# Optimization experiments

Measured on AMD Instinct MI355X. Metric: run time of the kernel, lower is better.

## Reference

```python
import jax, jax.numpy as jnp
import numpy as np
from jax import lax

B, IN_CH, H, W = 512, 20, 32, 32
FEAT, NUM_AGENTS, NUM_ACTIONS = 128, 4, 16
NUM_UNIT, NUM_CITY = 12, 4


def setup_inputs() -> dict:
    key = jax.random.key(0)
    ks = jax.random.split(key, 6)
    states = jax.random.normal(ks[0], (B, IN_CH, H, W), dtype=jnp.float32)
    labels = jax.random.randint(ks[1], (B,), 0, NUM_AGENTS, dtype=jnp.int32)
    maskings = jnp.ones((B, 1, H, W), dtype=jnp.float32)
    # get_feature params: 3x3 conv trunk (stand-in for PolicyNetwork.get_feature)
    conv_w = jax.random.normal(ks[2], (FEAT, IN_CH, 3, 3), dtype=jnp.float32) * 0.05
    conv_b = jnp.zeros((FEAT,), dtype=jnp.float32)
    # Stacked per-agent heads: index 0 = policy_net.fc1, 1.. = fc_list
    W_all = jax.random.normal(ks[3], (NUM_AGENTS, NUM_ACTIONS, FEAT), dtype=jnp.float32) * 0.05
    b_all = jax.random.normal(ks[4], (NUM_AGENTS, NUM_ACTIONS), dtype=jnp.float32) * 0.05
    return {"states": states, "labels": labels, "maskings": maskings,
            "conv_w": conv_w, "conv_b": conv_b, "W_all": W_all, "b_all": b_all}


def _get_feature(states, maskings, conv_w, conv_b):
    x = lax.conv_general_dilated(states, conv_w, (1, 1), 'SAME',
                                 dimension_numbers=('NCHW', 'OIHW', 'NCHW'))
    x = jax.nn.relu(x + conv_b[None, :, None, None])
    return x * maskings  # [B, FEAT, H, W]


def reference(states, labels, maskings, conv_w, conv_b, W_all, b_all):
    x = _get_feature(states, maskings, conv_w, conv_b)
    b, c, h, w = x.shape
    x = x.transpose(0, 2, 3, 1).reshape(b, h * w, c)  # [B, HW, C]
    # Equivalent to computing all num_agents heads then gathering by label:
    # select each sample's head weights, then one batched GEMM.
    W_sel = W_all[labels]          # [B, K, C]
    b_sel = b_all[labels]          # [B, K]
    out = jnp.einsum('bnc,bkc->bnk', x, W_sel) + b_sel[:, None, :]
    out = out.reshape(b, h, w, NUM_ACTIONS)
    return out[..., :NUM_UNIT], out[..., NUM_UNIT:]
```

## Files before the change

kernel.cpp:

```cpp
#include <hip/hip_runtime.h>
#include <hip/hip_bf16.h>
#include <stdint.h>

#define BATCH   512
#define INCH    20
#define FEAT    128
#define KACT    16
#define NUNIT   12

typedef short bf16x8 __attribute__((ext_vector_type(8)));
typedef float f32x4  __attribute__((ext_vector_type(4)));

#define BPACK_ELEMS (3*2*4*128*8)
#define WHEAD_ELEMS (4*4*4*16*8)

#define XIN_ELEMS   (34*34*20 + 64)

__device__ __forceinline__ uint16_t f2bf(float f) {
    union { float f; uint32_t u; } x{f};
    uint32_t u = x.u;
    return (uint16_t)((u + 0x7FFFu + ((u >> 16) & 1u)) >> 16);
}

__device__ __forceinline__ uint32_t cvt_pk_bf16(float lo, float hi) {
    uint32_t r;
    asm("v_cvt_pk_bf16_f32 %0, %1, %2" : "=v"(r) : "v"(lo), "v"(hi));
    return r;
}

__device__ __forceinline__ void lds_barrier() {
    asm volatile("s_waitcnt lgkmcnt(0)\n\ts_barrier" ::: "memory");
}

__global__ void repack_kernel(const float* __restrict__ conv_w,
                              const float* __restrict__ W_all,
                              uint16_t* __restrict__ Bpack,
                              uint16_t* __restrict__ Whead) {
    int idx = blockIdx.x * 256 + threadIdx.x;
    if (idx < BPACK_ELEMS) {
        int j = idx & 7, t = idx >> 3;
        int f = t & 127; t >>= 7;
        int g = t & 3;   t >>= 2;
        int kk = t & 1;  int ky = t >> 1;
        int k = kk * 32 + g * 8 + j;
        float v = 0.0f;
        if (k < 60) {
            int kx = k / 20, c = k % 20;
            v = conv_w[((f * INCH + c) * 3 + ky) * 3 + kx];
        }
        Bpack[idx] = f2bf(v);
    } else if (idx < BPACK_ELEMS + WHEAD_ELEMS) {
        int i = idx - BPACK_ELEMS;
        int j = i & 7, t = i >> 3;
        int a = t & 15; t >>= 4;
        int g = t & 3;  t >>= 2;
        int kt = t & 3; int ag = t >> 2;
        int f = kt * 32 + g * 8 + j;
        Whead[i] = f2bf(W_all[(ag * KACT + a) * FEAT + f]);
    }
}

__global__ __launch_bounds__(512, 4) void fused_mfma_kernel(
    const float* __restrict__ states,
    const int*   __restrict__ labels,
    const float* __restrict__ maskings,
    const float* __restrict__ conv_b,
    const float* __restrict__ b_all,
    const uint16_t* __restrict__ Bpack,
    const uint16_t* __restrict__ Whead,
    float*       __restrict__ out)
{
    __shared__ __align__(16) uint16_t xin[XIN_ELEMS];
    __shared__ __align__(16) uint16_t xl[2 * 64 * 128];

    const int b    = blockIdx.x;
    const int tid  = threadIdx.x;
    const int lane = tid & 63;
    const int w    = tid >> 6;
    const int l15  = lane & 15;
    const int g    = lane >> 4;
    const int wr   = w >> 2;
    const int fq   = w & 3;
    const int swz  = (l15 & 7) << 4;

    for (int i = tid; i < XIN_ELEMS / 8; i += 512)
        ((uint4*)xin)[i] = uint4{0, 0, 0, 0};
    __syncthreads();

    for (int t = 0; t < 10; ++t) {
        int i  = t * 512 + tid;
        int p  = i & 1023;
        int cg = i >> 10;
        int y  = p >> 5, x = p & 31;
        const float* sp = states + (size_t)b * (INCH * 1024) + cg * 4096 + p;
        float v0 = sp[0], v1 = sp[1024], v2 = sp[2048], v3 = sp[3072];
        uint64_t lo = cvt_pk_bf16(v0, v1);
        uint64_t hi = cvt_pk_bf16(v2, v3);
        *(uint64_t*)&xin[((y + 1) * 34 + (x + 1)) * 20 + cg * 4] = lo | (hi << 32);
    }

    const int label = labels[b];
    f32x4 cb[2];
    #pragma unroll
    for (int nt = 0; nt < 2; ++nt)
        cb[nt] = *(const f32x4*)&conv_b[fq * 32 + nt * 16 + g * 4];
    const f32x4 hb = *(const f32x4*)&b_all[label * KACT + g * 4];
    bf16x8 Wh[4];
    #pragma unroll
    for (int kt = 0; kt < 4; ++kt)
        Wh[kt] = *(const bf16x8*)&Whead[(((label * 4 + kt) * 4 + g) * 16 + l15) * 8];

    bf16x8 Wc[3][2][2];
    #pragma unroll
    for (int ky = 0; ky < 3; ++ky)
        #pragma unroll
        for (int kk = 0; kk < 2; ++kk)
            #pragma unroll
            for (int nt = 0; nt < 2; ++nt)
                Wc[ky][kk][nt] = *(const bf16x8*)
                    &Bpack[((((ky * 2 + kk) * 4 + g) * 128 + fq * 32 + nt * 16 + l15) * 8)];

    const int hoff0 = ((wr * 2 + fq) * 16 + l15) * 256;
    const bool do_head = (fq < 2);

    __syncthreads();

    #pragma unroll 2
    for (int s = 0; s < 16; ++s) {
        const int y = s * 2 + wr;

        const float m0 = maskings[(size_t)b * 1024 + y * 32 + l15];
        const float m1 = maskings[(size_t)b * 1024 + y * 32 + 16 + l15];

        f32x4 acc[2][2];
        #pragma unroll
        for (int pt = 0; pt < 2; ++pt)
            #pragma unroll
            for (int nt = 0; nt < 2; ++nt)
                acc[pt][nt] = f32x4{0.f, 0.f, 0.f, 0.f};

        __builtin_amdgcn_s_setprio(1);
        #pragma unroll
        for (int ky = 0; ky < 3; ++ky) {
            const uint64_t* a0 = (const uint64_t*)&xin[((y + ky) * 34 + l15) * 20 + g * 8];
            const uint64_t* a1 = (const uint64_t*)&xin[((y + ky) * 34 + 16 + l15) * 20 + g * 8];
            #pragma unroll
            for (int kk = 0; kk < 2; ++kk) {
                union { uint64_t u[2]; bf16x8 v; } B0, B1;
                B0.u[0] = a0[kk * 8 + 0]; B0.u[1] = a0[kk * 8 + 1];
                B1.u[0] = a1[kk * 8 + 0]; B1.u[1] = a1[kk * 8 + 1];
                #pragma unroll
                for (int nt = 0; nt < 2; ++nt) {
                    acc[0][nt] = __builtin_amdgcn_mfma_f32_16x16x32_bf16(
                        Wc[ky][kk][nt], B0.v, acc[0][nt], 0, 0, 0);
                    acc[1][nt] = __builtin_amdgcn_mfma_f32_16x16x32_bf16(
                        Wc[ky][kk][nt], B1.v, acc[1][nt], 0, 0, 0);
                }
            }
        }
        __builtin_amdgcn_s_setprio(0);

        char* xbase = (char*)xl + (s & 1) * 16384;
        #pragma unroll
        for (int pt = 0; pt < 2; ++pt) {
            const float m = pt ? m1 : m0;
            #pragma unroll
            for (int nt = 0; nt < 2; ++nt) {
                float x0 = fmaxf(acc[pt][nt][0] + cb[nt][0], 0.f) * m;
                float x1 = fmaxf(acc[pt][nt][1] + cb[nt][1], 0.f) * m;
                float x2 = fmaxf(acc[pt][nt][2] + cb[nt][2], 0.f) * m;
                float x3 = fmaxf(acc[pt][nt][3] + cb[nt][3], 0.f) * m;
                uint64_t pk = (uint64_t)cvt_pk_bf16(x0, x1)
                            | ((uint64_t)cvt_pk_bf16(x2, x3) << 32);
                const int off = ((wr * 2 + pt) * 16 + l15) * 256 + fq * 64 + nt * 32 + g * 8;
                *(uint64_t*)(xbase + (off ^ swz)) = pk;
            }
        }

        lds_barrier();

        if (do_head) {
            f32x4 hacc = f32x4{0.f, 0.f, 0.f, 0.f};
            __builtin_amdgcn_s_setprio(1);
            #pragma unroll
            for (int kt = 0; kt < 4; ++kt) {
                const int off = hoff0 + kt * 64 + g * 16;
                bf16x8 bx = *(const bf16x8*)(xbase + (off ^ swz));
                hacc = __builtin_amdgcn_mfma_f32_16x16x32_bf16(Wh[kt], bx, hacc, 0, 0, 0);
            }
            __builtin_amdgcn_s_setprio(0);
            const size_t pos = (size_t)b * 1024 + y * 32 + fq * 16 + l15;
            f32x4 o = hacc + hb;
            if (g < 3) *(f32x4*)&out[pos * NUNIT + g * 4] = o;
            else       *(f32x4*)&out[(size_t)BATCH * 1024 * NUNIT + pos * 4] = o;
        }
    }
}

extern "C" void kernel_launch(void* const* d_in, const int* in_sizes, int n_in,
                              void* d_out, int out_size, void* d_ws, size_t ws_size,
                              hipStream_t stream) {
    const float* states   = (const float*)d_in[0];
    const int*   labels   = (const int*)d_in[1];
    const float* maskings = (const float*)d_in[2];
    const float* conv_w   = (const float*)d_in[3];
    const float* conv_b   = (const float*)d_in[4];
    const float* W_all    = (const float*)d_in[5];
    const float* b_all    = (const float*)d_in[6];
    float* out = (float*)d_out;

    uint16_t* Bpack = (uint16_t*)d_ws;
    uint16_t* Whead = Bpack + BPACK_ELEMS;

    repack_kernel<<<(BPACK_ELEMS + WHEAD_ELEMS + 255) / 256, 256, 0, stream>>>(
        conv_w, W_all, Bpack, Whead);
    fused_mfma_kernel<<<BATCH, 512, 0, stream>>>(
        states, labels, maskings, conv_b, b_all, Bpack, Whead, out);
}
```

Baseline: 41.30 us.

## Switch conv to 32x32x16 MFMA and split each image into half-row blocks

The conv trunk now uses 32x32x16 bf16 MFMA tiles, with each wave covering 32 pixels by 64 features and the conv bias preloaded into the accumulators. The grid doubles to two 256-thread blocks per image, each staging only 18 padded rows. This is meant to raise MFMA efficiency, cut per-block LDS footprint and padding work, and spread work across more blocks. The trade-offs are heavier register use from the 16-wide accumulators and 24 weight fragments per lane, plus a halo row loaded twice.

```diff
diff --git a/kernel.cpp b/kernel.cpp
--- a/kernel.cpp
+++ b/kernel.cpp
@@ -10,11 +10,13 @@
 
 typedef short bf16x8 __attribute__((ext_vector_type(8)));
 typedef float f32x4  __attribute__((ext_vector_type(4)));
-
-#define BPACK_ELEMS (3*2*4*128*8)
+typedef float f32x16 __attribute__((ext_vector_type(16)));
+
+#define WPACK_ELEMS (3*4*2*128*8)
 #define WHEAD_ELEMS (4*4*4*16*8)
 
-#define XIN_ELEMS   (34*34*20 + 64)
+#define XIN_ROWS  18
+#define XIN_ELEMS (XIN_ROWS*34*20 + 64)
 
 __device__ __forceinline__ uint16_t f2bf(float f) {
     union { float f; uint32_t u; } x{f};
@@ -34,23 +36,23 @@
 
 __global__ void repack_kernel(const float* __restrict__ conv_w,
                               const float* __restrict__ W_all,
-                              uint16_t* __restrict__ Bpack,
+                              uint16_t* __restrict__ Wpack,
                               uint16_t* __restrict__ Whead) {
     int idx = blockIdx.x * 256 + threadIdx.x;
-    if (idx < BPACK_ELEMS) {
+    if (idx < WPACK_ELEMS) {
         int j = idx & 7, t = idx >> 3;
         int f = t & 127; t >>= 7;
-        int g = t & 3;   t >>= 2;
-        int kk = t & 1;  int ky = t >> 1;
-        int k = kk * 32 + g * 8 + j;
+        int h = t & 1;   t >>= 1;
+        int ks = t & 3;  int ky = t >> 2;
+        int k = ks * 16 + h * 8 + j;
         float v = 0.0f;
         if (k < 60) {
             int kx = k / 20, c = k % 20;
             v = conv_w[((f * INCH + c) * 3 + ky) * 3 + kx];
         }
-        Bpack[idx] = f2bf(v);
-    } else if (idx < BPACK_ELEMS + WHEAD_ELEMS) {
-        int i = idx - BPACK_ELEMS;
+        Wpack[idx] = f2bf(v);
+    } else if (idx < WPACK_ELEMS + WHEAD_ELEMS) {
+        int i = idx - WPACK_ELEMS;
         int j = i & 7, t = i >> 3;
         int a = t & 15; t >>= 4;
         int g = t & 3;  t >>= 2;
@@ -60,136 +62,142 @@
     }
 }
 
-__global__ __launch_bounds__(512, 4) void fused_mfma_kernel(
+__global__ __launch_bounds__(256, 2) void fused_mfma_kernel(
     const float* __restrict__ states,
     const int*   __restrict__ labels,
     const float* __restrict__ maskings,
     const float* __restrict__ conv_b,
     const float* __restrict__ b_all,
-    const uint16_t* __restrict__ Bpack,
+    const uint16_t* __restrict__ Wpack,
     const uint16_t* __restrict__ Whead,
     float*       __restrict__ out)
 {
     __shared__ __align__(16) uint16_t xin[XIN_ELEMS];
     __shared__ __align__(16) uint16_t xl[2 * 64 * 128];
 
-    const int b    = blockIdx.x;
+    const int bid  = blockIdx.x;
+    const int b    = bid >> 1;
+    const int y0   = (bid & 1) << 4;
     const int tid  = threadIdx.x;
     const int lane = tid & 63;
     const int w    = tid >> 6;
+    const int fh   = w >> 1;
+    const int rp   = w & 1;
+    const int l31  = lane & 31;
+    const int h    = lane >> 5;
     const int l15  = lane & 15;
     const int g    = lane >> 4;
-    const int wr   = w >> 2;
-    const int fq   = w & 3;
-    const int swz  = (l15 & 7) << 4;
-
-    for (int i = tid; i < XIN_ELEMS / 8; i += 512)
+
+    for (int i = tid; i < (XIN_ELEMS * 2) / 16; i += 256)
         ((uint4*)xin)[i] = uint4{0, 0, 0, 0};
     __syncthreads();
 
-    for (int t = 0; t < 10; ++t) {
-        int i  = t * 512 + tid;
-        int p  = i & 1023;
-        int cg = i >> 10;
-        int y  = p >> 5, x = p & 31;
-        const float* sp = states + (size_t)b * (INCH * 1024) + cg * 4096 + p;
-        float v0 = sp[0], v1 = sp[1024], v2 = sp[2048], v3 = sp[3072];
-        uint64_t lo = cvt_pk_bf16(v0, v1);
-        uint64_t hi = cvt_pk_bf16(v2, v3);
-        *(uint64_t*)&xin[((y + 1) * 34 + (x + 1)) * 20 + cg * 4] = lo | (hi << 32);
+    for (int t = 0; t < 12; ++t) {
+        int i = t * 256 + tid;
+        if (i < XIN_ROWS * 5 * 32) {
+            int p  = i & 31;
+            int tt = i >> 5;
+            int cg = tt % 5;
+            int r  = tt / 5;
+            int y  = y0 + r - 1;
+            if (y >= 0 && y < 32) {
+                const float* sp = states + (size_t)b * (INCH * 1024) + cg * 4096 + y * 32 + p;
+                float v0 = sp[0], v1 = sp[1024], v2 = sp[2048], v3 = sp[3072];
+                uint64_t lo = cvt_pk_bf16(v0, v1);
+                uint64_t hi = cvt_pk_bf16(v2, v3);
+                *(uint64_t*)&xin[(r * 34 + p + 1) * 20 + cg * 4] = lo | (hi << 32);
+            }
+        }
     }
 
     const int label = labels[b];
-    f32x4 cb[2];
+
+    f32x16 accI[2];
     #pragma unroll
     for (int nt = 0; nt < 2; ++nt)
-        cb[nt] = *(const f32x4*)&conv_b[fq * 32 + nt * 16 + g * 4];
+        #pragma unroll
+        for (int q = 0; q < 4; ++q) {
+            f32x4 c4 = *(const f32x4*)&conv_b[fh * 64 + nt * 32 + q * 8 + h * 4];
+            #pragma unroll
+            for (int e = 0; e < 4; ++e) accI[nt][q * 4 + e] = c4[e];
+        }
+
     const f32x4 hb = *(const f32x4*)&b_all[label * KACT + g * 4];
     bf16x8 Wh[4];
     #pragma unroll
     for (int kt = 0; kt < 4; ++kt)
         Wh[kt] = *(const bf16x8*)&Whead[(((label * 4 + kt) * 4 + g) * 16 + l15) * 8];
 
-    bf16x8 Wc[3][2][2];
+    bf16x8 Wc[2][3][4];
     #pragma unroll
-    for (int ky = 0; ky < 3; ++ky)
-        #pragma unroll
-        for (int kk = 0; kk < 2; ++kk)
-            #pragma unroll
-            for (int nt = 0; nt < 2; ++nt)
-                Wc[ky][kk][nt] = *(const bf16x8*)
-                    &Bpack[((((ky * 2 + kk) * 4 + g) * 128 + fq * 32 + nt * 16 + l15) * 8)];
-
-    const int hoff0 = ((wr * 2 + fq) * 16 + l15) * 256;
-    const bool do_head = (fq < 2);
+    for (int nt = 0; nt < 2; ++nt)
+        #pragma unroll
+        for (int ky = 0; ky < 3; ++ky)
+            #pragma unroll
+            for (int ks = 0; ks < 4; ++ks)
+                Wc[nt][ky][ks] = *(const bf16x8*)
+                    &Wpack[((((ky * 4 + ks) * 2 + h) * 128 + fh * 64 + nt * 32 + l31) * 8)];
+
+    const int posx  = rp * 32 + l31;
+    const int wswz  = (posx & 7) << 4;
+    const int hoff0 = (w * 16 + l15) * 256;
+    const int hswz  = (l15 & 7) << 4;
 
     __syncthreads();
 
     #pragma unroll 2
-    for (int s = 0; s < 16; ++s) {
-        const int y = s * 2 + wr;
-
-        const float m0 = maskings[(size_t)b * 1024 + y * 32 + l15];
-        const float m1 = maskings[(size_t)b * 1024 + y * 32 + 16 + l15];
-
-        f32x4 acc[2][2];
-        #pragma unroll
-        for (int pt = 0; pt < 2; ++pt)
-            #pragma unroll
-            for (int nt = 0; nt < 2; ++nt)
-                acc[pt][nt] = f32x4{0.f, 0.f, 0.f, 0.f};
+    for (int s = 0; s < 8; ++s) {
+        const int lr = 2 * s + rp;
+
+        const float m = maskings[(size_t)b * 1024 + (y0 + lr) * 32 + l31];
+
+        f32x16 acc0 = accI[0];
+        f32x16 acc1 = accI[1];
 
         __builtin_amdgcn_s_setprio(1);
         #pragma unroll
         for (int ky = 0; ky < 3; ++ky) {
-            const uint64_t* a0 = (const uint64_t*)&xin[((y + ky) * 34 + l15) * 20 + g * 8];
-            const uint64_t* a1 = (const uint64_t*)&xin[((y + ky) * 34 + 16 + l15) * 20 + g * 8];
-            #pragma unroll
-            for (int kk = 0; kk < 2; ++kk) {
-                union { uint64_t u[2]; bf16x8 v; } B0, B1;
-                B0.u[0] = a0[kk * 8 + 0]; B0.u[1] = a0[kk * 8 + 1];
-                B1.u[0] = a1[kk * 8 + 0]; B1.u[1] = a1[kk * 8 + 1];
-                #pragma unroll
-                for (int nt = 0; nt < 2; ++nt) {
-                    acc[0][nt] = __builtin_amdgcn_mfma_f32_16x16x32_bf16(
-                        Wc[ky][kk][nt], B0.v, acc[0][nt], 0, 0, 0);
-                    acc[1][nt] = __builtin_amdgcn_mfma_f32_16x16x32_bf16(
-                        Wc[ky][kk][nt], B1.v, acc[1][nt], 0, 0, 0);
-                }
+            const char* rbase = (const char*)xin + (((lr + ky) * 34 + l31) * 20 + h * 8) * 2;
+            #pragma unroll
+            for (int ks = 0; ks < 4; ++ks) {
+                bf16x8 X = *(const bf16x8*)(rbase + ks * 32);
+                acc0 = __builtin_amdgcn_mfma_f32_32x32x16_bf16(Wc[0][ky][ks], X, acc0, 0, 0, 0);
+                acc1 = __builtin_amdgcn_mfma_f32_32x32x16_bf16(Wc[1][ky][ks], X, acc1, 0, 0, 0);
             }
         }
         __builtin_amdgcn_s_setprio(0);
 
         char* xbase = (char*)xl + (s & 1) * 16384;
         #pragma unroll
-        for (int pt = 0; pt < 2; ++pt) {
-            const float m = pt ? m1 : m0;
-            #pragma unroll
-            for (int nt = 0; nt < 2; ++nt) {
-                float x0 = fmaxf(acc[pt][nt][0] + cb[nt][0], 0.f) * m;
-                float x1 = fmaxf(acc[pt][nt][1] + cb[nt][1], 0.f) * m;
-                float x2 = fmaxf(acc[pt][nt][2] + cb[nt][2], 0.f) * m;
-                float x3 = fmaxf(acc[pt][nt][3] + cb[nt][3], 0.f) * m;
+        for (int nt = 0; nt < 2; ++nt) {
+            const f32x16 A = nt ? acc1 : acc0;
+            #pragma unroll
+            for (int q = 0; q < 4; ++q) {
+                float x0 = fmaxf(A[q * 4 + 0], 0.f) * m;
+                float x1 = fmaxf(A[q * 4 + 1], 0.f) * m;
+                float x2 = fmaxf(A[q * 4 + 2], 0.f) * m;
+                float x3 = fmaxf(A[q * 4 + 3], 0.f) * m;
                 uint64_t pk = (uint64_t)cvt_pk_bf16(x0, x1)
                             | ((uint64_t)cvt_pk_bf16(x2, x3) << 32);
-                const int off = ((wr * 2 + pt) * 16 + l15) * 256 + fq * 64 + nt * 32 + g * 8;
-                *(uint64_t*)(xbase + (off ^ swz)) = pk;
+                const int off = posx * 256 + fh * 128 + nt * 64 + q * 16 + h * 8;
+                *(uint64_t*)(xbase + (off ^ wswz)) = pk;
             }
         }
 
         lds_barrier();
 
-        if (do_head) {
+        {
             f32x4 hacc = f32x4{0.f, 0.f, 0.f, 0.f};
             __builtin_amdgcn_s_setprio(1);
             #pragma unroll
             for (int kt = 0; kt < 4; ++kt) {
                 const int off = hoff0 + kt * 64 + g * 16;
-                bf16x8 bx = *(const bf16x8*)(xbase + (off ^ swz));
+                bf16x8 bx = *(const bf16x8*)(xbase + (off ^ hswz));
                 hacc = __builtin_amdgcn_mfma_f32_16x16x32_bf16(Wh[kt], bx, hacc, 0, 0, 0);
             }
             __builtin_amdgcn_s_setprio(0);
-            const size_t pos = (size_t)b * 1024 + y * 32 + fq * 16 + l15;
+            const int y = y0 + 2 * s + (w >> 1);
+            const size_t pos = (size_t)b * 1024 + y * 32 + (w & 1) * 16 + l15;
             f32x4 o = hacc + hb;
             if (g < 3) *(f32x4*)&out[pos * NUNIT + g * 4] = o;
             else       *(f32x4*)&out[(size_t)BATCH * 1024 * NUNIT + pos * 4] = o;
@@ -209,11 +217,11 @@
     const float* b_all    = (const float*)d_in[6];
     float* out = (float*)d_out;
 
-    uint16_t* Bpack = (uint16_t*)d_ws;
-    uint16_t* Whead = Bpack + BPACK_ELEMS;
-
-    repack_kernel<<<(BPACK_ELEMS + WHEAD_ELEMS + 255) / 256, 256, 0, stream>>>(
-        conv_w, W_all, Bpack, Whead);
-    fused_mfma_kernel<<<BATCH, 512, 0, stream>>>(
-        states, labels, maskings, conv_b, b_all, Bpack, Whead, out);
-}
+    uint16_t* Wpack = (uint16_t*)d_ws;
+    uint16_t* Whead = Wpack + WPACK_ELEMS;
+
+    repack_kernel<<<(WPACK_ELEMS + WHEAD_ELEMS + 255) / 256, 256, 0, stream>>>(
+        conv_w, W_all, Wpack, Whead);
+    fused_mfma_kernel<<<BATCH * 2, 256, 0, stream>>>(
+        states, labels, maskings, conv_b, b_all, Wpack, Whead, out);
+}
```

After: 72.57 us. 1.76x slower.

## Split each sample into four 8-row blocks with 4-wave workgroups

Applied to the files above, without the earlier changes.

The grid now has four blocks per sample, each covering 8 output rows, and each block has 256 threads instead of 512. Each block stages only a 10-row haloed input slab in LDS. Each wave computes 64 feature channels over 4 MFMA tiles instead of 32 over 2, and all four waves run the head GEMM, with head weights read from LDS and two accumulators. The aim is better load balance and occupancy with a smaller LDS footprint per block. In exchange, about 25% of the input rows (the halos) are reloaded and each thread holds more weight registers.

```diff
diff --git a/kernel.cpp b/kernel.cpp
--- a/kernel.cpp
+++ b/kernel.cpp
@@ -14,7 +14,8 @@
 #define BPACK_ELEMS (3*2*4*128*8)
 #define WHEAD_ELEMS (4*4*4*16*8)
 
-#define XIN_ELEMS   (34*34*20 + 64)
+#define XIN_ROWS  10
+#define XIN_ELEMS (XIN_ROWS*34*20 + 64)
 
 __device__ __forceinline__ uint16_t f2bf(float f) {
     union { float f; uint32_t u; } x{f};
@@ -60,7 +61,7 @@
     }
 }
 
-__global__ __launch_bounds__(512, 4) void fused_mfma_kernel(
+__global__ __launch_bounds__(256, 3) void fused_mfma_kernel(
     const float* __restrict__ states,
     const int*   __restrict__ labels,
     const float* __restrict__ maskings,
@@ -72,125 +73,133 @@
 {
     __shared__ __align__(16) uint16_t xin[XIN_ELEMS];
     __shared__ __align__(16) uint16_t xl[2 * 64 * 128];
-
-    const int b    = blockIdx.x;
+    __shared__ __align__(16) uint16_t whl[4 * 4 * 16 * 8];
+
+    const int bid  = blockIdx.x;
+    const int b    = bid >> 2;
+    const int y0   = (bid & 3) << 3;
     const int tid  = threadIdx.x;
     const int lane = tid & 63;
     const int w    = tid >> 6;
+    const int wr   = w & 1;
+    const int fh   = w >> 1;
     const int l15  = lane & 15;
     const int g    = lane >> 4;
-    const int wr   = w >> 2;
-    const int fq   = w & 3;
     const int swz  = (l15 & 7) << 4;
 
-    for (int i = tid; i < XIN_ELEMS / 8; i += 512)
+    for (int i = tid; i < (XIN_ELEMS * 2) / 16; i += 256)
         ((uint4*)xin)[i] = uint4{0, 0, 0, 0};
     __syncthreads();
 
-    for (int t = 0; t < 10; ++t) {
-        int i  = t * 512 + tid;
-        int p  = i & 1023;
-        int cg = i >> 10;
-        int y  = p >> 5, x = p & 31;
-        const float* sp = states + (size_t)b * (INCH * 1024) + cg * 4096 + p;
-        float v0 = sp[0], v1 = sp[1024], v2 = sp[2048], v3 = sp[3072];
-        uint64_t lo = cvt_pk_bf16(v0, v1);
-        uint64_t hi = cvt_pk_bf16(v2, v3);
-        *(uint64_t*)&xin[((y + 1) * 34 + (x + 1)) * 20 + cg * 4] = lo | (hi << 32);
-    }
-
     const int label = labels[b];
-    f32x4 cb[2];
+
+    for (int t = 0; t < 7; ++t) {
+        int i = t * 256 + tid;
+        if (i < XIN_ROWS * 5 * 32) {
+            int p  = i & 31;
+            int tt = i >> 5;
+            int cg = tt % 5;
+            int r  = tt / 5;
+            int y  = y0 + r - 1;
+            if (y >= 0 && y < 32) {
+                const float* sp = states + (size_t)b * (INCH * 1024) + cg * 4096 + y * 32 + p;
+                float v0 = sp[0], v1 = sp[1024], v2 = sp[2048], v3 = sp[3072];
+                uint64_t lo = cvt_pk_bf16(v0, v1);
+                uint64_t hi = cvt_pk_bf16(v2, v3);
+                *(uint64_t*)&xin[(r * 34 + p + 1) * 20 + cg * 4] = lo | (hi << 32);
+            }
+        }
+    }
+    {
+        *(bf16x8*)&whl[tid * 8] = *(const bf16x8*)&Whead[(label * 256 + tid) * 8];
+    }
+
+    f32x4 cb[4];
     #pragma unroll
-    for (int nt = 0; nt < 2; ++nt)
-        cb[nt] = *(const f32x4*)&conv_b[fq * 32 + nt * 16 + g * 4];
+    for (int nt = 0; nt < 4; ++nt)
+        cb[nt] = *(const f32x4*)&conv_b[fh * 64 + nt * 16 + g * 4];
     const f32x4 hb = *(const f32x4*)&b_all[label * KACT + g * 4];
-    bf16x8 Wh[4];
-    #pragma unroll
-    for (int kt = 0; kt < 4; ++kt)
-        Wh[kt] = *(const bf16x8*)&Whead[(((label * 4 + kt) * 4 + g) * 16 + l15) * 8];
-
-    bf16x8 Wc[3][2][2];
+
+    bf16x8 Wc[3][2][4];
     #pragma unroll
     for (int ky = 0; ky < 3; ++ky)
         #pragma unroll
         for (int kk = 0; kk < 2; ++kk)
             #pragma unroll
-            for (int nt = 0; nt < 2; ++nt)
+            for (int nt = 0; nt < 4; ++nt)
                 Wc[ky][kk][nt] = *(const bf16x8*)
-                    &Bpack[((((ky * 2 + kk) * 4 + g) * 128 + fq * 32 + nt * 16 + l15) * 8)];
-
-    const int hoff0 = ((wr * 2 + fq) * 16 + l15) * 256;
-    const bool do_head = (fq < 2);
+                    &Bpack[((((ky * 2 + kk) * 4 + g) * 128 + fh * 64 + nt * 16 + l15) * 8)];
+
+    const int hoff0 = (w * 16 + l15) * 256;
 
     __syncthreads();
 
     #pragma unroll 2
-    for (int s = 0; s < 16; ++s) {
-        const int y = s * 2 + wr;
+    for (int s = 0; s < 4; ++s) {
+        const int lr = 2 * s + wr;
+        const int y  = y0 + lr;
 
         const float m0 = maskings[(size_t)b * 1024 + y * 32 + l15];
         const float m1 = maskings[(size_t)b * 1024 + y * 32 + 16 + l15];
 
-        f32x4 acc[2][2];
-        #pragma unroll
-        for (int pt = 0; pt < 2; ++pt)
-            #pragma unroll
-            for (int nt = 0; nt < 2; ++nt)
-                acc[pt][nt] = f32x4{0.f, 0.f, 0.f, 0.f};
+        char* xbase = (char*)xl + (s & 1) * 16384;
 
         __builtin_amdgcn_s_setprio(1);
         #pragma unroll
-        for (int ky = 0; ky < 3; ++ky) {
-            const uint64_t* a0 = (const uint64_t*)&xin[((y + ky) * 34 + l15) * 20 + g * 8];
-            const uint64_t* a1 = (const uint64_t*)&xin[((y + ky) * 34 + 16 + l15) * 20 + g * 8];
-            #pragma unroll
-            for (int kk = 0; kk < 2; ++kk) {
-                union { uint64_t u[2]; bf16x8 v; } B0, B1;
-                B0.u[0] = a0[kk * 8 + 0]; B0.u[1] = a0[kk * 8 + 1];
-                B1.u[0] = a1[kk * 8 + 0]; B1.u[1] = a1[kk * 8 + 1];
+        for (int pt = 0; pt < 2; ++pt) {
+            f32x4 acc[4];
+            #pragma unroll
+            for (int nt = 0; nt < 4; ++nt) acc[nt] = f32x4{0.f, 0.f, 0.f, 0.f};
+
+            #pragma unroll
+            for (int ky = 0; ky < 3; ++ky) {
+                const uint64_t* ap = (const uint64_t*)
+                    &xin[((lr + ky) * 34 + pt * 16 + l15) * 20 + g * 8];
                 #pragma unroll
-                for (int nt = 0; nt < 2; ++nt) {
-                    acc[0][nt] = __builtin_amdgcn_mfma_f32_16x16x32_bf16(
-                        Wc[ky][kk][nt], B0.v, acc[0][nt], 0, 0, 0);
-                    acc[1][nt] = __builtin_amdgcn_mfma_f32_16x16x32_bf16(
-                        Wc[ky][kk][nt], B1.v, acc[1][nt], 0, 0, 0);
+                for (int kk = 0; kk < 2; ++kk) {
+                    union { uint64_t u[2]; bf16x8 v; } B;
+                    B.u[0] = ap[kk * 8 + 0];
+                    B.u[1] = ap[kk * 8 + 1];
+                    #pragma unroll
+                    for (int nt = 0; nt < 4; ++nt)
+                        acc[nt] = __builtin_amdgcn_mfma_f32_16x16x32_bf16(
+                            Wc[ky][kk][nt], B.v, acc[nt], 0, 0, 0);
                 }
             }
-        }
-        __builtin_amdgcn_s_setprio(0);
-
-        char* xbase = (char*)xl + (s & 1) * 16384;
-        #pragma unroll
-        for (int pt = 0; pt < 2; ++pt) {
+
             const float m = pt ? m1 : m0;
             #pragma unroll
-            for (int nt = 0; nt < 2; ++nt) {
-                float x0 = fmaxf(acc[pt][nt][0] + cb[nt][0], 0.f) * m;
-                float x1 = fmaxf(acc[pt][nt][1] + cb[nt][1], 0.f) * m;
-                float x2 = fmaxf(acc[pt][nt][2] + cb[nt][2], 0.f) * m;
-                float x3 = fmaxf(acc[pt][nt][3] + cb[nt][3], 0.f) * m;
+            for (int nt = 0; nt < 4; ++nt) {
+                float x0 = fmaxf(acc[nt][0] + cb[nt][0], 0.f) * m;
+                float x1 = fmaxf(acc[nt][1] + cb[nt][1], 0.f) * m;
+                float x2 = fmaxf(acc[nt][2] + cb[nt][2], 0.f) * m;
+                float x3 = fmaxf(acc[nt][3] + cb[nt][3], 0.f) * m;
                 uint64_t pk = (uint64_t)cvt_pk_bf16(x0, x1)
                             | ((uint64_t)cvt_pk_bf16(x2, x3) << 32);
-                const int off = ((wr * 2 + pt) * 16 + l15) * 256 + fq * 64 + nt * 32 + g * 8;
+                const int off = ((wr * 2 + pt) * 16 + l15) * 256 + fh * 128 + nt * 32 + g * 8;
                 *(uint64_t*)(xbase + (off ^ swz)) = pk;
             }
         }
+        __builtin_amdgcn_s_setprio(0);
 
         lds_barrier();
 
-        if (do_head) {
-            f32x4 hacc = f32x4{0.f, 0.f, 0.f, 0.f};
+        {
+            f32x4 h0 = f32x4{0.f, 0.f, 0.f, 0.f};
+            f32x4 h1 = f32x4{0.f, 0.f, 0.f, 0.f};
             __builtin_amdgcn_s_setprio(1);
             #pragma unroll
             for (int kt = 0; kt < 4; ++kt) {
+                bf16x8 wh = *(const bf16x8*)&whl[((kt * 4 + g) * 16 + l15) * 8];
                 const int off = hoff0 + kt * 64 + g * 16;
                 bf16x8 bx = *(const bf16x8*)(xbase + (off ^ swz));
-                hacc = __builtin_amdgcn_mfma_f32_16x16x32_bf16(Wh[kt], bx, hacc, 0, 0, 0);
+                if (kt & 1) h1 = __builtin_amdgcn_mfma_f32_16x16x32_bf16(wh, bx, h1, 0, 0, 0);
+                else        h0 = __builtin_amdgcn_mfma_f32_16x16x32_bf16(wh, bx, h0, 0, 0, 0);
             }
             __builtin_amdgcn_s_setprio(0);
-            const size_t pos = (size_t)b * 1024 + y * 32 + fq * 16 + l15;
-            f32x4 o = hacc + hb;
+            const int hy = y0 + 2 * s + (w >> 1);
+            const size_t pos = (size_t)b * 1024 + hy * 32 + (w & 1) * 16 + l15;
+            f32x4 o = h0 + h1 + hb;
             if (g < 3) *(f32x4*)&out[pos * NUNIT + g * 4] = o;
             else       *(f32x4*)&out[(size_t)BATCH * 1024 * NUNIT + pos * 4] = o;
         }
@@ -214,6 +223,6 @@
 
     repack_kernel<<<(BPACK_ELEMS + WHEAD_ELEMS + 255) / 256, 256, 0, stream>>>(
         conv_w, W_all, Bpack, Whead);
-    fused_mfma_kernel<<<BATCH, 512, 0, stream>>>(
+    fused_mfma_kernel<<<BATCH * 4, 256, 0, stream>>>(
         states, labels, maskings, conv_b, b_all, Bpack, Whead, out);
 }
```

Result: slower. 54.40 us (+31.7%).

## Split each image into four 8-row strips per block with halo loading

Applied to the files above, without the earlier changes.

Each block now handles one 8-row strip of an image with 256 threads, instead of a whole image with 512 threads. The grid grows fourfold and shared memory per block shrinks a lot, since the input tile holds only 10 padded rows and the feature buffer is halved. This is meant to raise occupancy and shorten the serial per-block row loop. The cost is that halo rows are loaded twice from global memory and the per-block setup (weight register loads, zeroing) runs four times as often.

```diff
diff --git a/kernel.cpp b/kernel.cpp
--- a/kernel.cpp
+++ b/kernel.cpp
@@ -14,7 +14,8 @@
 #define BPACK_ELEMS (3*2*4*128*8)
 #define WHEAD_ELEMS (4*4*4*16*8)
 
-#define XIN_ELEMS   (34*34*20 + 64)
+#define XIN_ROWS  10
+#define XIN_ELEMS (XIN_ROWS*34*20 + 64)
 
 __device__ __forceinline__ uint16_t f2bf(float f) {
     union { float f; uint32_t u; } x{f};
@@ -60,7 +61,7 @@
     }
 }
 
-__global__ __launch_bounds__(512, 4) void fused_mfma_kernel(
+__global__ __launch_bounds__(256, 4) void fused_mfma_kernel(
     const float* __restrict__ states,
     const int*   __restrict__ labels,
     const float* __restrict__ maskings,
@@ -71,32 +72,38 @@
     float*       __restrict__ out)
 {
     __shared__ __align__(16) uint16_t xin[XIN_ELEMS];
-    __shared__ __align__(16) uint16_t xl[2 * 64 * 128];
-
-    const int b    = blockIdx.x;
+    __shared__ __align__(16) uint16_t xl[2 * 32 * 128];
+
+    const int bid  = blockIdx.x;
+    const int b    = bid >> 2;
+    const int y0   = (bid & 3) << 3;
     const int tid  = threadIdx.x;
     const int lane = tid & 63;
-    const int w    = tid >> 6;
+    const int fq   = tid >> 6;
     const int l15  = lane & 15;
     const int g    = lane >> 4;
-    const int wr   = w >> 2;
-    const int fq   = w & 3;
     const int swz  = (l15 & 7) << 4;
 
-    for (int i = tid; i < XIN_ELEMS / 8; i += 512)
+    for (int i = tid; i < (XIN_ELEMS * 2) / 16; i += 256)
         ((uint4*)xin)[i] = uint4{0, 0, 0, 0};
     __syncthreads();
 
-    for (int t = 0; t < 10; ++t) {
-        int i  = t * 512 + tid;
-        int p  = i & 1023;
-        int cg = i >> 10;
-        int y  = p >> 5, x = p & 31;
-        const float* sp = states + (size_t)b * (INCH * 1024) + cg * 4096 + p;
-        float v0 = sp[0], v1 = sp[1024], v2 = sp[2048], v3 = sp[3072];
-        uint64_t lo = cvt_pk_bf16(v0, v1);
-        uint64_t hi = cvt_pk_bf16(v2, v3);
-        *(uint64_t*)&xin[((y + 1) * 34 + (x + 1)) * 20 + cg * 4] = lo | (hi << 32);
+    for (int t = 0; t < 7; ++t) {
+        int i = t * 256 + tid;
+        if (i < XIN_ROWS * 5 * 32) {
+            int p  = i & 31;
+            int tt = i >> 5;
+            int cg = tt % 5;
+            int r  = tt / 5;
+            int y  = y0 + r - 1;
+            if (y >= 0 && y < 32) {
+                const float* sp = states + (size_t)b * (INCH * 1024) + cg * 4096 + y * 32 + p;
+                float v0 = sp[0], v1 = sp[1024], v2 = sp[2048], v3 = sp[3072];
+                uint64_t lo = cvt_pk_bf16(v0, v1);
+                uint64_t hi = cvt_pk_bf16(v2, v3);
+                *(uint64_t*)&xin[(r * 34 + p + 1) * 20 + cg * 4] = lo | (hi << 32);
+            }
+        }
     }
 
     const int label = labels[b];
@@ -120,14 +127,14 @@
                 Wc[ky][kk][nt] = *(const bf16x8*)
                     &Bpack[((((ky * 2 + kk) * 4 + g) * 128 + fq * 32 + nt * 16 + l15) * 8)];
 
-    const int hoff0 = ((wr * 2 + fq) * 16 + l15) * 256;
+    const int hoff0 = (fq * 16 + l15) * 256;
     const bool do_head = (fq < 2);
 
     __syncthreads();
 
     #pragma unroll 2
-    for (int s = 0; s < 16; ++s) {
-        const int y = s * 2 + wr;
+    for (int s = 0; s < 8; ++s) {
+        const int y = y0 + s;
 
         const float m0 = maskings[(size_t)b * 1024 + y * 32 + l15];
         const float m1 = maskings[(size_t)b * 1024 + y * 32 + 16 + l15];
@@ -142,8 +149,8 @@
         __builtin_amdgcn_s_setprio(1);
         #pragma unroll
         for (int ky = 0; ky < 3; ++ky) {
-            const uint64_t* a0 = (const uint64_t*)&xin[((y + ky) * 34 + l15) * 20 + g * 8];
-            const uint64_t* a1 = (const uint64_t*)&xin[((y + ky) * 34 + 16 + l15) * 20 + g * 8];
+            const uint64_t* a0 = (const uint64_t*)&xin[((s + ky) * 34 + l15) * 20 + g * 8];
+            const uint64_t* a1 = (const uint64_t*)&xin[((s + ky) * 34 + 16 + l15) * 20 + g * 8];
             #pragma unroll
             for (int kk = 0; kk < 2; ++kk) {
                 union { uint64_t u[2]; bf16x8 v; } B0, B1;
@@ -160,7 +167,7 @@
         }
         __builtin_amdgcn_s_setprio(0);
 
-        char* xbase = (char*)xl + (s & 1) * 16384;
+        char* xbase = (char*)xl + (s & 1) * 8192;
         #pragma unroll
         for (int pt = 0; pt < 2; ++pt) {
             const float m = pt ? m1 : m0;
@@ -172,7 +179,7 @@
                 float x3 = fmaxf(acc[pt][nt][3] + cb[nt][3], 0.f) * m;
                 uint64_t pk = (uint64_t)cvt_pk_bf16(x0, x1)
                             | ((uint64_t)cvt_pk_bf16(x2, x3) << 32);
-                const int off = ((wr * 2 + pt) * 16 + l15) * 256 + fq * 64 + nt * 32 + g * 8;
+                const int off = (pt * 16 + l15) * 256 + fq * 64 + nt * 32 + g * 8;
                 *(uint64_t*)(xbase + (off ^ swz)) = pk;
             }
         }
@@ -214,6 +221,6 @@
 
     repack_kernel<<<(BPACK_ELEMS + WHEAD_ELEMS + 255) / 256, 256, 0, stream>>>(
         conv_w, W_all, Bpack, Whead);
-    fused_mfma_kernel<<<BATCH, 512, 0, stream>>>(
+    fused_mfma_kernel<<<BATCH * 4, 256, 0, stream>>>(
         states, labels, maskings, conv_b, b_all, Bpack, Whead, out);
 }
```

After: 42.15 us. 2.1% more time.
